# Optimization experiments

Measured on AMD Instinct MI355X. Metric: run time of the kernel, lower is better.

## Reference

```python
import jax, jax.numpy as jnp
import numpy as np

B, S, D, H = 2, 2048, 1024, 16
HD = D // H  # head size 64

def setup_inputs() -> dict:
    key = jax.random.key(0)
    ks = jax.random.split(key, 7)
    sc = 1.0 / np.sqrt(D)
    return {
        "batch_data": jax.random.normal(ks[0], (B, S, D), dtype=jnp.float32),
        "Wq": jax.random.normal(ks[1], (D, D), dtype=jnp.float32) * sc,
        "bq": jnp.zeros((D,), dtype=jnp.float32),
        "Wk": jax.random.normal(ks[2], (D, D), dtype=jnp.float32) * sc,
        "bk": jnp.zeros((D,), dtype=jnp.float32),
        "Wv": jax.random.normal(ks[3], (D, D), dtype=jnp.float32) * sc,
        "bv": jnp.zeros((D,), dtype=jnp.float32),
    }

def _split_heads(x):
    # [B,S,D] -> [B,H,S,HD]
    b, s, _ = x.shape
    return x.reshape(b, s, H, HD).transpose(0, 2, 1, 3)

def reference(batch_data, Wq, bq, Wk, bk, Wv, bv):
    q = _split_heads(batch_data @ Wq + bq)
    k = _split_heads(batch_data @ Wk + bk)
    v = _split_heads(batch_data @ Wv + bv)
    scores = jnp.einsum('bhqd,bhkd->bhqk', q, k) / jnp.sqrt(jnp.float32(HD))
    probs = jax.nn.softmax(scores, axis=-1)
    ctx = jnp.einsum('bhqk,bhkd->bhqd', probs, v)  # [B,H,S,HD]
    ctx = ctx.transpose(0, 2, 1, 3).reshape(batch_data.shape[0], batch_data.shape[1], D)
    return jnp.mean(ctx, axis=1)  # mean pool over sequence -> [B,D]
```

## Files before the change

### kernel.cpp

```cpp
#include <hip/hip_runtime.h>
#include <hip/hip_bf16.h>
#include <stdint.h>

#define B_  2
#define S_  2048
#define D_  1024
#define H_  16
#define HD_ 64

typedef __attribute__((ext_vector_type(8))) __bf16 bf16x8;
typedef __attribute__((ext_vector_type(4))) __bf16 bf16x4;
typedef __attribute__((ext_vector_type(4))) float  f32x4;

__device__ __forceinline__ __bf16 f2bf(float f) {
  union { float f; uint32_t u; } v; v.f = f;
  uint32_t r = v.u + 0x7FFF + ((v.u >> 16) & 1);
  unsigned short h = (unsigned short)(r >> 16);
  return __builtin_bit_cast(__bf16, h);
}

__device__ __forceinline__ void gload16(const void* g, void* l) {
  __builtin_amdgcn_global_load_lds(
      (__attribute__((address_space(1))) void*)(uintptr_t)g,
      (__attribute__((address_space(3))) void*)(uintptr_t)l,
      16, 0, 0);
}

__global__ __launch_bounds__(256) void zero_out_k(float* out) {
  int i = blockIdx.x * 256 + threadIdx.x;
  if (i < B_ * D_) out[i] = 0.0f;
}

__global__ __launch_bounds__(256) void convert_x(const float* __restrict__ x,
                                                 __bf16* __restrict__ xb) {
  int i = blockIdx.x * 256 + threadIdx.x;
  float4 v = ((const float4*)x)[i];
  bf16x4 o;
  o[0] = f2bf(v.x); o[1] = f2bf(v.y); o[2] = f2bf(v.z); o[3] = f2bf(v.w);
  ((bf16x4*)xb)[i] = o;
}

__global__ __launch_bounds__(256) void transpose_w(const float* __restrict__ wq,
                                                   const float* __restrict__ wk,
                                                   const float* __restrict__ wv,
                                                   __bf16* __restrict__ wt) {
  __shared__ float tile[32][33];
  const float* w = (blockIdx.z == 0) ? wq : (blockIdx.z == 1 ? wk : wv);
  __bf16* o = wt + (size_t)blockIdx.z * D_ * D_;
  int k0 = blockIdx.y * 32, n0 = blockIdx.x * 32;
  int tx = threadIdx.x, ty = threadIdx.y;
  for (int i = 0; i < 4; ++i)
    tile[ty + 8 * i][tx] = w[(size_t)(k0 + ty + 8 * i) * D_ + n0 + tx];
  __syncthreads();
  for (int i = 0; i < 4; ++i)
    o[(size_t)(n0 + ty + 8 * i) * D_ + k0 + tx] = f2bf(tile[tx][ty + 8 * i]);
}

__global__ __launch_bounds__(256, 2) void gemm_qkv(
    const __bf16* __restrict__ xb, const __bf16* __restrict__ wt,
    const float* __restrict__ bq, const float* __restrict__ bk,
    const float* __restrict__ bv, __bf16* __restrict__ qh,
    __bf16* __restrict__ kh, __bf16* __restrict__ vt) {
  constexpr int K = 1024;
  __shared__ __attribute__((aligned(16))) __bf16 lA[128 * 32];
  __shared__ __attribute__((aligned(16))) __bf16 lB[128 * 32];

  const int z = blockIdx.z;
  const __bf16* w = wt + (size_t)z * K * D_;
  const float* bias = (z == 0) ? bq : (z == 1 ? bk : bv);
  const int t = threadIdx.x;
  const int lane = t & 63;
  const int wid = t >> 6;
  const int quad = lane >> 4;
  const int col = lane & 15;
  const int m0 = blockIdx.y * 128;
  const int n0 = blockIdx.x * 128;
  const int wr = (wid >> 1) * 64;
  const int wc = (wid & 1) * 64;

  const int srow = t >> 2;
  const int gc = (t & 3) ^ ((t >> 3) & 3);

  f32x4 acc[4][4] = {};

  for (int kt = 0; kt < K / 32; ++kt) {
    __syncthreads();
    for (int r2 = 0; r2 < 2; ++r2) {
      int row = r2 * 64 + srow;
      gload16(xb + (size_t)(m0 + row) * K + kt * 32 + gc * 8,
              (char*)lA + row * 64 + (t & 3) * 16);
      gload16(w + (size_t)(n0 + row) * K + kt * 32 + gc * 8,
              (char*)lB + row * 64 + (t & 3) * 16);
    }
    __syncthreads();

    bf16x8 afrag[4], bfrag[4];
    for (int mi = 0; mi < 4; ++mi) {
      int m = wr + mi * 16 + col;
      int ch = quad ^ ((m >> 1) & 3);
      afrag[mi] = *(const bf16x8*)((const char*)lA + m * 64 + ch * 16);
    }
    for (int ni = 0; ni < 4; ++ni) {
      int n = wc + ni * 16 + col;
      int ch = quad ^ ((n >> 1) & 3);
      bfrag[ni] = *(const bf16x8*)((const char*)lB + n * 64 + ch * 16);
    }
    for (int mi = 0; mi < 4; ++mi)
      for (int ni = 0; ni < 4; ++ni)
        acc[mi][ni] = __builtin_amdgcn_mfma_f32_16x16x32_bf16(
            afrag[mi], bfrag[ni], acc[mi][ni], 0, 0, 0);
  }

  for (int mi = 0; mi < 4; ++mi) {
    for (int ni = 0; ni < 4; ++ni) {
      int gn = n0 + wc + ni * 16 + col;
      float bi = bias[gn];
      int h = gn >> 6, hd = gn & 63;
      for (int r = 0; r < 4; ++r) {
        int gm = m0 + wr + mi * 16 + quad * 4 + r;
        int b = gm >> 11, s = gm & 2047;
        float v = acc[mi][ni][r] + bi;
        if (z < 2) {
          __bf16* dst = (z == 0) ? qh : kh;
          dst[((size_t)(b * H_ + h) * S_ + s) * HD_ + hd] = f2bf(v);
        } else {
          vt[((size_t)(b * H_ + h) * HD_ + hd) * S_ + s] = f2bf(v);
        }
      }
    }
  }
}

__global__ __launch_bounds__(256, 2) void attn(const __bf16* __restrict__ qh,
                                               const __bf16* __restrict__ kh,
                                               const __bf16* __restrict__ vt,
                                               float* __restrict__ out) {
  __shared__ __attribute__((aligned(16))) __bf16 lK[128 * 64];
  __shared__ __attribute__((aligned(16))) __bf16 lV[64 * 128];
  __shared__ __attribute__((aligned(16))) __bf16 lP[4][32 * 128];

  const int t = threadIdx.x;
  const int lane = t & 63;
  const int wid = t >> 6;
  const int quad = lane >> 4;
  const int col = lane & 15;
  const int bh = blockIdx.y;
  const int q0 = blockIdx.x * 128 + wid * 32;

  const __bf16* qbase = qh + (size_t)bh * S_ * HD_;
  const __bf16* kbase = kh + (size_t)bh * S_ * HD_;
  const __bf16* vbase = vt + (size_t)bh * HD_ * S_;

  bf16x8 aq[2][2];
  for (int mi = 0; mi < 2; ++mi)
    for (int ks = 0; ks < 2; ++ks)
      aq[mi][ks] = *(const bf16x8*)(qbase + (size_t)(q0 + mi * 16 + col) * HD_ +
                                    ks * 32 + quad * 8);

  f32x4 o[2][4] = {};
  float l_state[2][4] = {};

  const int krow = t >> 3;
  const int kgc = (t & 7) ^ ((t >> 3) & 7);
  const int vrow = t >> 4;
  const int vgc = (t & 15) ^ ((t >> 4) & 15);

  const float scale = 0.125f;

  for (int kt = 0; kt < S_ / 128; ++kt) {
    __syncthreads();
    for (int r2 = 0; r2 < 4; ++r2) {
      int row = r2 * 32 + krow;
      gload16(kbase + (size_t)(kt * 128 + row) * HD_ + kgc * 8,
              (char*)lK + row * 128 + (t & 7) * 16);
      int rowv = r2 * 16 + vrow;
      gload16(vbase + (size_t)rowv * S_ + kt * 128 + vgc * 8,
              (char*)lV + rowv * 256 + (t & 15) * 16);
    }
    __syncthreads();

    f32x4 sc[2][8] = {};
    for (int ks = 0; ks < 2; ++ks) {
      for (int nk = 0; nk < 8; ++nk) {
        int row = nk * 16 + col;
        int c = ks * 4 + quad;
        int ch = c ^ (row & 7);
        bf16x8 bkf = *(const bf16x8*)((const char*)lK + row * 128 + ch * 16);
        for (int mi = 0; mi < 2; ++mi)
          sc[mi][nk] = __builtin_amdgcn_mfma_f32_16x16x32_bf16(
              aq[mi][ks], bkf, sc[mi][nk], 0, 0, 0);
      }
    }

    for (int mi = 0; mi < 2; ++mi) {
      float rs[4] = {0.f, 0.f, 0.f, 0.f};
      for (int nk = 0; nk < 8; ++nk) {
        for (int r = 0; r < 4; ++r) {
          float e = __expf(sc[mi][nk][r] * scale);
          __bf16 pb = f2bf(e);
          int row = mi * 16 + quad * 4 + r;
          int byteoff = nk * 32 + col * 2;
          int c = byteoff >> 4;
          int ch = c ^ (row & 15);
          *((__bf16*)((char*)&lP[wid][0] + row * 256 + ch * 16 + (byteoff & 15))) = pb;
          rs[r] += (float)pb;
        }
      }
      for (int r = 0; r < 4; ++r) {
        float v = rs[r];
        v += __shfl_xor(v, 1);  v += __shfl_xor(v, 2);
        v += __shfl_xor(v, 4);  v += __shfl_xor(v, 8);
        l_state[mi][r] += v;
      }
    }

    for (int ks2 = 0; ks2 < 4; ++ks2) {
      bf16x8 ap[2];
      for (int mi = 0; mi < 2; ++mi) {
        int row = mi * 16 + col;
        int c = ks2 * 4 + quad;
        int ch = c ^ (row & 15);
        ap[mi] = *(const bf16x8*)((const char*)&lP[wid][0] + row * 256 + ch * 16);
      }
      for (int nj = 0; nj < 4; ++nj) {
        int rowv2 = nj * 16 + col;
        int c2 = ks2 * 4 + quad;
        int ch2 = c2 ^ (rowv2 & 15);
        bf16x8 bvf = *(const bf16x8*)((const char*)lV + rowv2 * 256 + ch2 * 16);
        for (int mi = 0; mi < 2; ++mi)
          o[mi][nj] = __builtin_amdgcn_mfma_f32_16x16x32_bf16(
              ap[mi], bvf, o[mi][nj], 0, 0, 0);
      }
    }
  }

  float inv_l[2][4];
  for (int mi = 0; mi < 2; ++mi)
    for (int r = 0; r < 4; ++r) inv_l[mi][r] = 1.0f / l_state[mi][r];
  const int b = bh >> 4;
  const int h = bh & 15;
  for (int nj = 0; nj < 4; ++nj) {
    float s = 0.f;
    for (int mi = 0; mi < 2; ++mi)
      for (int r = 0; r < 4; ++r) s += o[mi][nj][r] * inv_l[mi][r];
    s += __shfl_xor(s, 16);
    s += __shfl_xor(s, 32);
    if (quad == 0)
      atomicAdd(out + (size_t)b * D_ + h * HD_ + nj * 16 + col, s * (1.0f / S_));
  }
}

extern "C" void kernel_launch(void* const* d_in, const int* in_sizes, int n_in,
                              void* d_out, int out_size, void* d_ws, size_t ws_size,
                              hipStream_t stream) {
  const float* x  = (const float*)d_in[0];
  const float* Wq = (const float*)d_in[1];
  const float* bq = (const float*)d_in[2];
  const float* Wk = (const float*)d_in[3];
  const float* bk = (const float*)d_in[4];
  const float* Wv = (const float*)d_in[5];
  const float* bv = (const float*)d_in[6];
  float* out = (float*)d_out;

  char* ws = (char*)d_ws;
  __bf16* xb = (__bf16*)(ws);
  __bf16* wt = (__bf16*)(ws + ((size_t)8  << 20));
  __bf16* qh = (__bf16*)(ws + ((size_t)14 << 20));
  __bf16* kh = (__bf16*)(ws + ((size_t)22 << 20));
  __bf16* vt = (__bf16*)(ws + ((size_t)30 << 20));

  zero_out_k<<<dim3((B_ * D_ + 255) / 256), dim3(256), 0, stream>>>(out);
  convert_x<<<dim3((B_ * S_ * D_) / 1024), dim3(256), 0, stream>>>(x, xb);
  transpose_w<<<dim3(32, 32, 3), dim3(32, 8), 0, stream>>>(Wq, Wk, Wv, wt);
  gemm_qkv<<<dim3(8, 32, 3), dim3(256), 0, stream>>>(xb, wt, bq, bk, bv, qh, kh, vt);
  attn<<<dim3(S_ / 128, B_ * H_), dim3(256), 0, stream>>>(qh, kh, vt, out);
}
```

Measured before the change: 191.3 us.

## Split attention over key chunks, fold scale into Q, vectorize GEMM epilogue stores

Attention is now split into two key-range halves (attn1) that write unnormalized partial outputs and row sums, and a second kernel (attn2) combines them and mean-pools. The softmax scale and log2(e) are folded into Q in the GEMM epilogue so exp2f can be used directly, and row sums are computed with an MFMA against a ones vector. The QKV GEMM swaps operand roles for Q/K so its epilogue can store packed bf16x4 vectors, and it uses hardware bf16 conversion casts with raised occupancy hints. This adds an extra kernel launch and an intermediate buffer round-trip, and like the code before it skips max subtraction in softmax.

```diff
diff --git a/kernel.cpp b/kernel.cpp
--- a/kernel.cpp
+++ b/kernel.cpp
@@ -12,12 +12,7 @@
 typedef __attribute__((ext_vector_type(4))) __bf16 bf16x4;
 typedef __attribute__((ext_vector_type(4))) float  f32x4;
 
-__device__ __forceinline__ __bf16 f2bf(float f) {
-  union { float f; uint32_t u; } v; v.f = f;
-  uint32_t r = v.u + 0x7FFF + ((v.u >> 16) & 1);
-  unsigned short h = (unsigned short)(r >> 16);
-  return __builtin_bit_cast(__bf16, h);
-}
+#define QSCALE 0.18033688011112042f
 
 __device__ __forceinline__ void gload16(const void* g, void* l) {
   __builtin_amdgcn_global_load_lds(
@@ -36,7 +31,7 @@
   int i = blockIdx.x * 256 + threadIdx.x;
   float4 v = ((const float4*)x)[i];
   bf16x4 o;
-  o[0] = f2bf(v.x); o[1] = f2bf(v.y); o[2] = f2bf(v.z); o[3] = f2bf(v.w);
+  o[0] = (__bf16)v.x; o[1] = (__bf16)v.y; o[2] = (__bf16)v.z; o[3] = (__bf16)v.w;
   ((bf16x4*)xb)[i] = o;
 }
 
@@ -53,10 +48,10 @@
     tile[ty + 8 * i][tx] = w[(size_t)(k0 + ty + 8 * i) * D_ + n0 + tx];
   __syncthreads();
   for (int i = 0; i < 4; ++i)
-    o[(size_t)(n0 + ty + 8 * i) * D_ + k0 + tx] = f2bf(tile[tx][ty + 8 * i]);
-}
-
-__global__ __launch_bounds__(256, 2) void gemm_qkv(
+    o[(size_t)(n0 + ty + 8 * i) * D_ + k0 + tx] = (__bf16)tile[tx][ty + 8 * i];
+}
+
+__global__ __launch_bounds__(256, 3) void gemm_qkv(
     const __bf16* __restrict__ xb, const __bf16* __restrict__ wt,
     const float* __restrict__ bq, const float* __restrict__ bk,
     const float* __restrict__ bv, __bf16* __restrict__ qh,
@@ -83,61 +78,102 @@
 
   f32x4 acc[4][4] = {};
 
-  for (int kt = 0; kt < K / 32; ++kt) {
-    __syncthreads();
-    for (int r2 = 0; r2 < 2; ++r2) {
-      int row = r2 * 64 + srow;
-      gload16(xb + (size_t)(m0 + row) * K + kt * 32 + gc * 8,
-              (char*)lA + row * 64 + (t & 3) * 16);
-      gload16(w + (size_t)(n0 + row) * K + kt * 32 + gc * 8,
-              (char*)lB + row * 64 + (t & 3) * 16);
-    }
-    __syncthreads();
-
-    bf16x8 afrag[4], bfrag[4];
-    for (int mi = 0; mi < 4; ++mi) {
-      int m = wr + mi * 16 + col;
-      int ch = quad ^ ((m >> 1) & 3);
-      afrag[mi] = *(const bf16x8*)((const char*)lA + m * 64 + ch * 16);
-    }
-    for (int ni = 0; ni < 4; ++ni) {
-      int n = wc + ni * 16 + col;
-      int ch = quad ^ ((n >> 1) & 3);
-      bfrag[ni] = *(const bf16x8*)((const char*)lB + n * 64 + ch * 16);
-    }
-    for (int mi = 0; mi < 4; ++mi)
-      for (int ni = 0; ni < 4; ++ni)
-        acc[mi][ni] = __builtin_amdgcn_mfma_f32_16x16x32_bf16(
-            afrag[mi], bfrag[ni], acc[mi][ni], 0, 0, 0);
+  if (z < 2) {
+    for (int kt = 0; kt < K / 32; ++kt) {
+      __syncthreads();
+      for (int r2 = 0; r2 < 2; ++r2) {
+        int row = r2 * 64 + srow;
+        gload16(xb + (size_t)(m0 + row) * K + kt * 32 + gc * 8,
+                (char*)lA + row * 64 + (t & 3) * 16);
+        gload16(w + (size_t)(n0 + row) * K + kt * 32 + gc * 8,
+                (char*)lB + row * 64 + (t & 3) * 16);
+      }
+      __syncthreads();
+      bf16x8 fw[4], fx[4];
+      for (int i = 0; i < 4; ++i) {
+        int n = wr + i * 16 + col;
+        int ch = quad ^ ((n >> 1) & 3);
+        fw[i] = *(const bf16x8*)((const char*)lB + n * 64 + ch * 16);
+      }
+      for (int j = 0; j < 4; ++j) {
+        int m = wc + j * 16 + col;
+        int ch = quad ^ ((m >> 1) & 3);
+        fx[j] = *(const bf16x8*)((const char*)lA + m * 64 + ch * 16);
+      }
+      for (int i = 0; i < 4; ++i)
+        for (int j = 0; j < 4; ++j)
+          acc[i][j] = __builtin_amdgcn_mfma_f32_16x16x32_bf16(
+              fw[i], fx[j], acc[i][j], 0, 0, 0);
+    }
+    const float scale = (z == 0) ? QSCALE : 1.0f;
+    __bf16* dst = (z == 0) ? qh : kh;
+    for (int i = 0; i < 4; ++i) {
+      int gnb = n0 + wr + i * 16 + quad * 4;
+      float4 bi = *(const float4*)(bias + gnb);
+      int h = gnb >> 6, hd = gnb & 63;
+      for (int j = 0; j < 4; ++j) {
+        int gm = m0 + wc + j * 16 + col;
+        int b = gm >> 11, s = gm & 2047;
+        bf16x4 pk;
+        pk[0] = (__bf16)((acc[i][j][0] + bi.x) * scale);
+        pk[1] = (__bf16)((acc[i][j][1] + bi.y) * scale);
+        pk[2] = (__bf16)((acc[i][j][2] + bi.z) * scale);
+        pk[3] = (__bf16)((acc[i][j][3] + bi.w) * scale);
+        *(bf16x4*)(dst + ((size_t)(b * H_ + h) * S_ + s) * HD_ + hd) = pk;
+      }
+    }
+  } else {
+    for (int kt = 0; kt < K / 32; ++kt) {
+      __syncthreads();
+      for (int r2 = 0; r2 < 2; ++r2) {
+        int row = r2 * 64 + srow;
+        gload16(xb + (size_t)(m0 + row) * K + kt * 32 + gc * 8,
+                (char*)lA + row * 64 + (t & 3) * 16);
+        gload16(w + (size_t)(n0 + row) * K + kt * 32 + gc * 8,
+                (char*)lB + row * 64 + (t & 3) * 16);
+      }
+      __syncthreads();
+      bf16x8 fx[4], fw[4];
+      for (int i = 0; i < 4; ++i) {
+        int m = wr + i * 16 + col;
+        int ch = quad ^ ((m >> 1) & 3);
+        fx[i] = *(const bf16x8*)((const char*)lA + m * 64 + ch * 16);
+      }
+      for (int j = 0; j < 4; ++j) {
+        int n = wc + j * 16 + col;
+        int ch = quad ^ ((n >> 1) & 3);
+        fw[j] = *(const bf16x8*)((const char*)lB + n * 64 + ch * 16);
+      }
+      for (int i = 0; i < 4; ++i)
+        for (int j = 0; j < 4; ++j)
+          acc[i][j] = __builtin_amdgcn_mfma_f32_16x16x32_bf16(
+              fx[i], fw[j], acc[i][j], 0, 0, 0);
+    }
+    for (int i = 0; i < 4; ++i) {
+      int gmb = m0 + wr + i * 16 + quad * 4;
+      int b = gmb >> 11, s = gmb & 2047;
+      for (int j = 0; j < 4; ++j) {
+        int gn = n0 + wc + j * 16 + col;
+        int h = gn >> 6, hd = gn & 63;
+        float bi = bias[gn];
+        bf16x4 pk;
+        pk[0] = (__bf16)(acc[i][j][0] + bi);
+        pk[1] = (__bf16)(acc[i][j][1] + bi);
+        pk[2] = (__bf16)(acc[i][j][2] + bi);
+        pk[3] = (__bf16)(acc[i][j][3] + bi);
+        *(bf16x4*)(vt + ((size_t)(b * H_ + h) * HD_ + hd) * S_ + s) = pk;
+      }
+    }
   }
-
-  for (int mi = 0; mi < 4; ++mi) {
-    for (int ni = 0; ni < 4; ++ni) {
-      int gn = n0 + wc + ni * 16 + col;
-      float bi = bias[gn];
-      int h = gn >> 6, hd = gn & 63;
-      for (int r = 0; r < 4; ++r) {
-        int gm = m0 + wr + mi * 16 + quad * 4 + r;
-        int b = gm >> 11, s = gm & 2047;
-        float v = acc[mi][ni][r] + bi;
-        if (z < 2) {
-          __bf16* dst = (z == 0) ? qh : kh;
-          dst[((size_t)(b * H_ + h) * S_ + s) * HD_ + hd] = f2bf(v);
-        } else {
-          vt[((size_t)(b * H_ + h) * HD_ + hd) * S_ + s] = f2bf(v);
-        }
-      }
-    }
-  }
-}
-
-__global__ __launch_bounds__(256, 2) void attn(const __bf16* __restrict__ qh,
-                                               const __bf16* __restrict__ kh,
-                                               const __bf16* __restrict__ vt,
-                                               float* __restrict__ out) {
-  __shared__ __attribute__((aligned(16))) __bf16 lK[128 * 64];
-  __shared__ __attribute__((aligned(16))) __bf16 lV[64 * 128];
-  __shared__ __attribute__((aligned(16))) __bf16 lP[4][32 * 128];
+}
+
+__global__ __launch_bounds__(256, 4) void attn1(
+    const __bf16* __restrict__ qh, const __bf16* __restrict__ kh,
+    const __bf16* __restrict__ vt, __bf16* __restrict__ po,
+    float* __restrict__ pl) {
+  __shared__ __attribute__((aligned(16))) __bf16 lK[64 * 64];
+  __shared__ __attribute__((aligned(16))) __bf16 lV[64 * 64];
+  __shared__ __attribute__((aligned(16))) __bf16 lP[4][32 * 64];
 
   const int t = threadIdx.x;
   const int lane = t & 63;
@@ -145,6 +181,7 @@
   const int quad = lane >> 4;
   const int col = lane & 15;
   const int bh = blockIdx.y;
+  const int kc = blockIdx.z;
   const int q0 = blockIdx.x * 128 + wid * 32;
 
   const __bf16* qbase = qh + (size_t)bh * S_ * HD_;
@@ -158,75 +195,62 @@
                                     ks * 32 + quad * 8);
 
   f32x4 o[2][4] = {};
-  float l_state[2][4] = {};
-
-  const int krow = t >> 3;
-  const int kgc = (t & 7) ^ ((t >> 3) & 7);
-  const int vrow = t >> 4;
-  const int vgc = (t & 15) ^ ((t >> 4) & 15);
-
-  const float scale = 0.125f;
-
-  for (int kt = 0; kt < S_ / 128; ++kt) {
+  f32x4 lacc[2] = {};
+
+  const int srow = t >> 3;
+  const int sgc = (t & 7) ^ ((t >> 3) & 7);
+  const int sslot = t & 7;
+
+  __bf16 oneb = (__bf16)1.0f;
+  bf16x8 ones = {oneb, oneb, oneb, oneb, oneb, oneb, oneb, oneb};
+
+  for (int kt = kc * 16; kt < kc * 16 + 16; ++kt) {
     __syncthreads();
-    for (int r2 = 0; r2 < 4; ++r2) {
-      int row = r2 * 32 + krow;
-      gload16(kbase + (size_t)(kt * 128 + row) * HD_ + kgc * 8,
-              (char*)lK + row * 128 + (t & 7) * 16);
-      int rowv = r2 * 16 + vrow;
-      gload16(vbase + (size_t)rowv * S_ + kt * 128 + vgc * 8,
-              (char*)lV + rowv * 256 + (t & 15) * 16);
+    for (int r2 = 0; r2 < 2; ++r2) {
+      int row = r2 * 32 + srow;
+      gload16(kbase + (size_t)(kt * 64 + row) * HD_ + sgc * 8,
+              (char*)lK + row * 128 + sslot * 16);
+      gload16(vbase + (size_t)row * S_ + kt * 64 + sgc * 8,
+              (char*)lV + row * 128 + sslot * 16);
     }
     __syncthreads();
 
-    f32x4 sc[2][8] = {};
-    for (int ks = 0; ks < 2; ++ks) {
-      for (int nk = 0; nk < 8; ++nk) {
+    f32x4 sc[2][4] = {};
+    for (int ks = 0; ks < 2; ++ks)
+      for (int nk = 0; nk < 4; ++nk) {
         int row = nk * 16 + col;
-        int c = ks * 4 + quad;
-        int ch = c ^ (row & 7);
+        int ch = (ks * 4 + quad) ^ (row & 7);
         bf16x8 bkf = *(const bf16x8*)((const char*)lK + row * 128 + ch * 16);
         for (int mi = 0; mi < 2; ++mi)
           sc[mi][nk] = __builtin_amdgcn_mfma_f32_16x16x32_bf16(
               aq[mi][ks], bkf, sc[mi][nk], 0, 0, 0);
       }
-    }
-
-    for (int mi = 0; mi < 2; ++mi) {
-      float rs[4] = {0.f, 0.f, 0.f, 0.f};
-      for (int nk = 0; nk < 8; ++nk) {
+
+    for (int mi = 0; mi < 2; ++mi)
+      for (int nk = 0; nk < 4; ++nk)
         for (int r = 0; r < 4; ++r) {
-          float e = __expf(sc[mi][nk][r] * scale);
-          __bf16 pb = f2bf(e);
-          int row = mi * 16 + quad * 4 + r;
+          float e = exp2f(sc[mi][nk][r]);
+          int rowp = mi * 16 + quad * 4 + r;
           int byteoff = nk * 32 + col * 2;
-          int c = byteoff >> 4;
-          int ch = c ^ (row & 15);
-          *((__bf16*)((char*)&lP[wid][0] + row * 256 + ch * 16 + (byteoff & 15))) = pb;
-          rs[r] += (float)pb;
+          int ch = (byteoff >> 4) ^ (rowp & 7);
+          *((__bf16*)((char*)&lP[wid][0] + rowp * 128 + ch * 16 +
+                      (byteoff & 15))) = (__bf16)e;
         }
-      }
-      for (int r = 0; r < 4; ++r) {
-        float v = rs[r];
-        v += __shfl_xor(v, 1);  v += __shfl_xor(v, 2);
-        v += __shfl_xor(v, 4);  v += __shfl_xor(v, 8);
-        l_state[mi][r] += v;
-      }
-    }
-
-    for (int ks2 = 0; ks2 < 4; ++ks2) {
+
+    for (int ks2 = 0; ks2 < 2; ++ks2) {
       bf16x8 ap[2];
       for (int mi = 0; mi < 2; ++mi) {
-        int row = mi * 16 + col;
-        int c = ks2 * 4 + quad;
-        int ch = c ^ (row & 15);
-        ap[mi] = *(const bf16x8*)((const char*)&lP[wid][0] + row * 256 + ch * 16);
-      }
+        int rowa = mi * 16 + col;
+        int ch = (ks2 * 4 + quad) ^ (rowa & 7);
+        ap[mi] = *(const bf16x8*)((const char*)&lP[wid][0] + rowa * 128 + ch * 16);
+      }
+      for (int mi = 0; mi < 2; ++mi)
+        lacc[mi] = __builtin_amdgcn_mfma_f32_16x16x32_bf16(
+            ap[mi], ones, lacc[mi], 0, 0, 0);
       for (int nj = 0; nj < 4; ++nj) {
-        int rowv2 = nj * 16 + col;
-        int c2 = ks2 * 4 + quad;
-        int ch2 = c2 ^ (rowv2 & 15);
-        bf16x8 bvf = *(const bf16x8*)((const char*)lV + rowv2 * 256 + ch2 * 16);
+        int rowv = nj * 16 + col;
+        int ch2 = (ks2 * 4 + quad) ^ (rowv & 7);
+        bf16x8 bvf = *(const bf16x8*)((const char*)lV + rowv * 128 + ch2 * 16);
         for (int mi = 0; mi < 2; ++mi)
           o[mi][nj] = __builtin_amdgcn_mfma_f32_16x16x32_bf16(
               ap[mi], bvf, o[mi][nj], 0, 0, 0);
@@ -234,19 +258,41 @@
     }
   }
 
-  float inv_l[2][4];
+  const size_t slab = (size_t)(kc * 32 + bh) * S_;
   for (int mi = 0; mi < 2; ++mi)
-    for (int r = 0; r < 4; ++r) inv_l[mi][r] = 1.0f / l_state[mi][r];
-  const int b = bh >> 4;
-  const int h = bh & 15;
-  for (int nj = 0; nj < 4; ++nj) {
-    float s = 0.f;
-    for (int mi = 0; mi < 2; ++mi)
-      for (int r = 0; r < 4; ++r) s += o[mi][nj][r] * inv_l[mi][r];
-    s += __shfl_xor(s, 16);
-    s += __shfl_xor(s, 32);
-    if (quad == 0)
-      atomicAdd(out + (size_t)b * D_ + h * HD_ + nj * 16 + col, s * (1.0f / S_));
+    for (int r = 0; r < 4; ++r) {
+      int qrow = q0 + mi * 16 + quad * 4 + r;
+      for (int nj = 0; nj < 4; ++nj)
+        po[(slab + qrow) * HD_ + nj * 16 + col] = (__bf16)o[mi][nj][r];
+      if (col == 0) pl[slab + qrow] = lacc[mi][r];
+    }
+}
+
+__global__ __launch_bounds__(256) void attn2(const __bf16* __restrict__ po,
+                                             const float* __restrict__ pl,
+                                             float* __restrict__ out) {
+  __shared__ float red[256];
+  const int t = threadIdx.x;
+  const int colhd = t & 63;
+  const int grp = t >> 6;
+  const int bh = blockIdx.y;
+  const int q0 = blockIdx.x * 128;
+  const size_t s0 = (size_t)bh * S_;
+  const size_t s1 = (size_t)(32 + bh) * S_;
+  float acc = 0.f;
+  for (int i = 0; i < 32; ++i) {
+    int row = q0 + grp * 32 + i;
+    float l = pl[s0 + row] + pl[s1 + row];
+    float v = (float)po[(s0 + row) * HD_ + colhd] +
+              (float)po[(s1 + row) * HD_ + colhd];
+    acc += v / l;
+  }
+  red[t] = acc;
+  __syncthreads();
+  if (t < 64) {
+    float s = red[t] + red[t + 64] + red[t + 128] + red[t + 192];
+    atomicAdd(out + (size_t)(bh >> 4) * D_ + (bh & 15) * HD_ + colhd,
+              s * (1.0f / S_));
   }
 }
 
@@ -263,15 +309,18 @@
   float* out = (float*)d_out;
 
   char* ws = (char*)d_ws;
-  __bf16* xb = (__bf16*)(ws);
-  __bf16* wt = (__bf16*)(ws + ((size_t)8  << 20));
-  __bf16* qh = (__bf16*)(ws + ((size_t)14 << 20));
-  __bf16* kh = (__bf16*)(ws + ((size_t)22 << 20));
-  __bf16* vt = (__bf16*)(ws + ((size_t)30 << 20));
+  __bf16* qh = (__bf16*)(ws);
+  __bf16* kh = (__bf16*)(ws + ((size_t)8  << 20));
+  __bf16* vt = (__bf16*)(ws + ((size_t)16 << 20));
+  __bf16* xb = (__bf16*)(ws + ((size_t)24 << 20));
+  __bf16* wt = (__bf16*)(ws + ((size_t)32 << 20));
+  __bf16* po = (__bf16*)(ws + ((size_t)24 << 20));
+  float*  pl = (float*) (ws + ((size_t)41 << 20));
 
   zero_out_k<<<dim3((B_ * D_ + 255) / 256), dim3(256), 0, stream>>>(out);
   convert_x<<<dim3((B_ * S_ * D_) / 1024), dim3(256), 0, stream>>>(x, xb);
   transpose_w<<<dim3(32, 32, 3), dim3(32, 8), 0, stream>>>(Wq, Wk, Wv, wt);
   gemm_qkv<<<dim3(8, 32, 3), dim3(256), 0, stream>>>(xb, wt, bq, bk, bv, qh, kh, vt);
-  attn<<<dim3(S_ / 128, B_ * H_), dim3(256), 0, stream>>>(qh, kh, vt, out);
-}
+  attn1<<<dim3(S_ / 128, B_ * H_, 2), dim3(256), 0, stream>>>(qh, kh, vt, po, pl);
+  attn2<<<dim3(S_ / 128, B_ * H_), dim3(256), 0, stream>>>(po, pl, out);
+}
```

After: 281.9 us. 47.3% more time.
